# Performance work log

Measured on AMD Instinct MI355X. Metric: run time of the kernel, lower is better.

The kernel has to match this reference:

```python
import jax, jax.numpy as jnp
import numpy as np

N_NODES = 50000
NEG_SLOPE = 0.2


def gat_layer(x, src, dst, edge_attr, W, a_src, a_dst, We, a_edge, b, n):
    """PyG GATConv (heads=1, concat=True, add_self_loops=True, fill_value='mean')."""
    h = x @ W                                   # [N, C] shared lin for src/dst
    alpha_s = h @ a_src                          # [N]
    alpha_d = h @ a_dst                          # [N]
    # self loops; self-loop edge_attr = mean of incoming edge_attr per node
    deg = jax.ops.segment_sum(jnp.ones_like(dst, dtype=edge_attr.dtype), dst, num_segments=n)
    ea_mean = jax.ops.segment_sum(edge_attr, dst, num_segments=n) / jnp.maximum(deg, 1.0)[:, None]
    loop = jnp.arange(n, dtype=src.dtype)
    s = jnp.concatenate([src, loop])             # [E+N]
    d = jnp.concatenate([dst, loop])
    ea = jnp.concatenate([edge_attr, ea_mean], axis=0)
    alpha_e = (ea @ We) @ a_edge                 # [E+N]
    alpha = jax.nn.leaky_relu(alpha_s[s] + alpha_d[d] + alpha_e, NEG_SLOPE)
    # segment softmax over destination neighborhoods (self-loops guarantee non-empty)
    amax = jax.ops.segment_max(alpha, d, num_segments=n)
    ealpha = jnp.exp(alpha - amax[d])
    denom = jax.ops.segment_sum(ealpha, d, num_segments=n)
    coef = ealpha / denom[d]                     # [E+N]
    out = jax.ops.segment_sum(h[s] * coef[:, None], d, num_segments=n)
    return out + b


def setup_inputs() -> dict:
    key = jax.random.key(0)
    ks = jax.random.split(key, 16)
    N, E, F_in, H, C, ED = N_NODES, 800000, 256, 128, 128, 60
    inp = {
        "x": jax.random.normal(ks[0], (N, F_in), jnp.float32),
        "edge_index": jax.random.randint(ks[1], (2, E), 0, N, jnp.int32),
        "edge_features": jax.random.normal(ks[2], (E, ED), jnp.float32),
        "batch_size": 16,
    }
    def glorot(k, shape):
        fan = shape[0] + (shape[1] if len(shape) > 1 else 1)
        return jax.random.normal(k, shape, jnp.float32) * np.sqrt(2.0 / fan)
    # layer 1
    inp["W1"] = glorot(ks[3], (F_in, H))
    inp["a_src1"] = glorot(ks[4], (H,))
    inp["a_dst1"] = glorot(ks[5], (H,))
    inp["We1"] = glorot(ks[6], (ED, H))
    inp["a_edge1"] = glorot(ks[7], (H,))
    inp["b1"] = jnp.zeros((H,), jnp.float32)
    # layer 2
    inp["W2"] = glorot(ks[8], (H, C))
    inp["a_src2"] = glorot(ks[9], (C,))
    inp["a_dst2"] = glorot(ks[10], (C,))
    inp["We2"] = glorot(ks[11], (ED, C))
    inp["a_edge2"] = glorot(ks[12], (C,))
    inp["b2"] = jnp.zeros((C,), jnp.float32)
    return inp


def reference(x, edge_index, edge_features, batch_size,
              W1, a_src1, a_dst1, We1, a_edge1, b1,
              W2, a_src2, a_dst2, We2, a_edge2, b2):
    n = x.shape[0]
    src, dst = edge_index[0], edge_index[1]
    h = gat_layer(x, src, dst, edge_features, W1, a_src1, a_dst1, We1, a_edge1, b1, n)
    h = jax.nn.relu(h)
    z = gat_layer(h, src, dst, edge_features, W2, a_src2, a_dst2, We2, a_edge2, b2, n)
    # decode: gather-dot over labeled edge pairs
    res = jnp.sum(z[src] * z[dst], axis=-1)      # [E]
    half = res.shape[0] // 2
    res_half = res[:half] + res[half:]
    return res_half.reshape((batch_size, -1))
```

## Files before the change

### kernel.cpp

```cpp
#include <hip/hip_runtime.h>
#include <hip/hip_bf16.h>

typedef __attribute__((ext_vector_type(8))) short short8;
typedef __attribute__((ext_vector_type(4))) float floatx4;

__device__ __forceinline__ float wsum(float v){
  #pragma unroll
  for (int m = 32; m >= 1; m >>= 1) v += __shfl_xor(v, m);
  return v;
}
__device__ __forceinline__ float lrelu(float a){ return a > 0.f ? a : 0.2f * a; }
__device__ __forceinline__ float bflo(unsigned u){ return __uint_as_float(u << 16); }
__device__ __forceinline__ float bfhi(unsigned u){ return __uint_as_float(u & 0xffff0000u); }
__device__ __forceinline__ unsigned short f2bf(float f){
  __hip_bfloat16 h = __float2bfloat16(f);
  return *reinterpret_cast<unsigned short*>(&h);
}

__global__ __launch_bounds__(256) void k_prep(const float* __restrict__ We1, const float* __restrict__ ae1,
                       const float* __restrict__ We2, const float* __restrict__ ae2,
                       float* __restrict__ we1, float* __restrict__ we2,
                       const float* __restrict__ W1, unsigned short* __restrict__ W1t,
                       const float* __restrict__ W2, unsigned short* __restrict__ W2t) {
  int b = blockIdx.x, t = threadIdx.x;
  if (b == 0) {
    if (t >= 64) return;
    float s1 = 0.f, s2 = 0.f;
    if (t < 60) {
      const float4* r1 = reinterpret_cast<const float4*>(We1 + t * 128);
      const float4* r2 = reinterpret_cast<const float4*>(We2 + t * 128);
      const float4* a1 = reinterpret_cast<const float4*>(ae1);
      const float4* a2 = reinterpret_cast<const float4*>(ae2);
      for (int i = 0; i < 32; ++i) {
        float4 x1 = r1[i], y1 = a1[i];
        float4 x2 = r2[i], y2 = a2[i];
        s1 += x1.x*y1.x + x1.y*y1.y + x1.z*y1.z + x1.w*y1.w;
        s2 += x2.x*y2.x + x2.y*y2.y + x2.z*y2.z + x2.w*y2.w;
      }
    }
    we1[t] = s1; we2[t] = s2;
  } else if (b <= 128) {
    int idx = (b - 1) * 256 + t;
    int k = idx >> 7, n = idx & 127;
    W1t[(size_t)n * 256 + k] = f2bf(W1[idx]);
  } else {
    int idx = (b - 129) * 256 + t;
    int k = idx >> 7, n = idx & 127;
    W2t[(size_t)n * 128 + k] = f2bf(W2[idx]);
  }
}

__global__ void k_count(const int* __restrict__ dst, int* __restrict__ degi,
                        int* __restrict__ eslot, int E) {
  int e = blockIdx.x * blockDim.x + threadIdx.x;
  if (e < E) eslot[e] = atomicAdd(degi + dst[e], 1);
}

__global__ __launch_bounds__(1024) void k_scan(const int* __restrict__ degi, int* __restrict__ rowptr,
                                               int N, int E) {
  __shared__ int part[1024];
  int t = threadIdx.x;
  const int CH = 52;
  int lo = t * CH;
  int v[52];
  int s = 0;
  #pragma unroll
  for (int i = 0; i < 13; ++i) {
    int base_i = lo + 4 * i;
    if (base_i + 4 <= N) {
      int4 q = *reinterpret_cast<const int4*>(degi + base_i);
      v[4*i+0] = q.x; v[4*i+1] = q.y; v[4*i+2] = q.z; v[4*i+3] = q.w;
      s += q.x + q.y + q.z + q.w;
    } else {
      #pragma unroll
      for (int j = 0; j < 4; ++j) {
        int idx = base_i + j;
        int x = (idx < N) ? degi[idx] : 0;
        v[4*i+j] = x; s += x;
      }
    }
  }
  part[t] = s;
  __syncthreads();
  for (int off = 1; off < 1024; off <<= 1) {
    int u = (t >= off) ? part[t - off] : 0;
    __syncthreads();
    part[t] += u;
    __syncthreads();
  }
  int base = (t == 0) ? 0 : part[t - 1];
  #pragma unroll
  for (int i = 0; i < 13; ++i) {
    int base_i = lo + 4 * i;
    if (base_i + 4 <= N) {
      int4 o;
      o.x = base; base += v[4*i+0];
      o.y = base; base += v[4*i+1];
      o.z = base; base += v[4*i+2];
      o.w = base; base += v[4*i+3];
      *reinterpret_cast<int4*>(rowptr + base_i) = o;
    } else {
      #pragma unroll
      for (int j = 0; j < 4; ++j) {
        int idx = base_i + j;
        if (idx < N) { rowptr[idx] = base; base += v[4*i+j]; }
      }
    }
  }
  if (t == 0) rowptr[N] = E;
}

__global__ __launch_bounds__(256) void k_fill(const int* __restrict__ src, const int* __restrict__ dst,
                       const float* __restrict__ ef,
                       const float* __restrict__ we1, const float* __restrict__ we2,
                       const int* __restrict__ rowptr, const int* __restrict__ eslot,
                       float4* __restrict__ csr, int E) {
  __shared__ float w1[64], w2[64];
  int t = threadIdx.x;
  if (t < 64) { w1[t] = we1[t]; w2[t] = we2[t]; }
  __syncthreads();
  int gid = blockIdx.x * 256 + t;
  int e = gid >> 2;
  int sub = gid & 3;
  if (e >= E) return;
  const float4* row = reinterpret_cast<const float4*>(ef + (size_t)e * 60);
  float d1 = 0.f, d2 = 0.f;
  #pragma unroll
  for (int i = sub; i < 15; i += 4) {
    float4 f = row[i];
    d1 += f.x*w1[4*i] + f.y*w1[4*i+1] + f.z*w1[4*i+2] + f.w*w1[4*i+3];
    d2 += f.x*w2[4*i] + f.y*w2[4*i+1] + f.z*w2[4*i+2] + f.w*w2[4*i+3];
  }
  d1 += __shfl_xor(d1, 1); d1 += __shfl_xor(d1, 2);
  d2 += __shfl_xor(d2, 1); d2 += __shfl_xor(d2, 2);
  if (sub == 0) {
    int d = dst[e];
    int slot = rowptr[d] + eslot[e];
    float4 v;
    v.x = __int_as_float(src[e]); v.y = d1; v.z = d2; v.w = 0.f;
    csr[slot] = v;
  }
}

template <int K, bool AFP32>
__global__ __launch_bounds__(256) void k_gemm(const void* __restrict__ Av, const unsigned short* __restrict__ Bt,
                                              unsigned short* __restrict__ C, int M) {
  int wid = (blockIdx.x * 256 + threadIdx.x) >> 6;
  int lane = threadIdx.x & 63;
  int mt = wid >> 1, hf = wid & 1;
  if (mt * 16 >= M) return;
  int r = lane & 15, quad = lane >> 4;
  int m = mt * 16 + r;
  floatx4 acc[4] = {};
  for (int k0 = 0; k0 < K; k0 += 32) {
    int kk = k0 + quad * 8;
    short8 a;
    if (AFP32) {
      const float4* ap = reinterpret_cast<const float4*>((const float*)Av + (size_t)m * K + kk);
      float4 lo = ap[0], hi = ap[1];
      union { short8 v; unsigned short u[8]; } pa;
      pa.u[0]=f2bf(lo.x); pa.u[1]=f2bf(lo.y); pa.u[2]=f2bf(lo.z); pa.u[3]=f2bf(lo.w);
      pa.u[4]=f2bf(hi.x); pa.u[5]=f2bf(hi.y); pa.u[6]=f2bf(hi.z); pa.u[7]=f2bf(hi.w);
      a = pa.v;
    } else {
      a = *reinterpret_cast<const short8*>((const unsigned short*)Av + (size_t)m * K + kk);
    }
    #pragma unroll
    for (int t = 0; t < 4; ++t) {
      short8 b = *reinterpret_cast<const short8*>(Bt + (size_t)(hf*64 + t*16 + r) * K + kk);
      acc[t] = __builtin_amdgcn_mfma_f32_16x16x32_bf16(a, b, acc[t], 0, 0, 0);
    }
  }
  #pragma unroll
  for (int t = 0; t < 4; ++t) {
    int col = hf * 64 + t * 16 + r;
    #pragma unroll
    for (int rr = 0; rr < 4; ++rr) {
      int row = mt * 16 + quad * 4 + rr;
      C[(size_t)row * 128 + col] = f2bf(acc[t][rr]);
    }
  }
}

__global__ void k_alpha(const unsigned short* __restrict__ h,
                        const float* __restrict__ a_src, const float* __restrict__ a_dst,
                        float* __restrict__ as_, float* __restrict__ ad_, int N) {
  int wave = (blockIdx.x * blockDim.x + threadIdx.x) >> 6;
  int lane = threadIdx.x & 63;
  if (wave >= N) return;
  unsigned u = *reinterpret_cast<const unsigned*>(h + (size_t)wave * 128 + lane * 2);
  float f0 = bflo(u), f1 = bfhi(u);
  float2 sv = reinterpret_cast<const float2*>(a_src)[lane];
  float2 dv = reinterpret_cast<const float2*>(a_dst)[lane];
  float ps = f0 * sv.x + f1 * sv.y;
  float pd = f0 * dv.x + f1 * dv.y;
  ps = wsum(ps);
  pd = wsum(pd);
  if (lane == 0) { as_[wave] = ps; ad_[wave] = pd; }
}

__global__ __launch_bounds__(256) void k_agg(const int* __restrict__ rowptr, const float4* __restrict__ csr,
                      const float* __restrict__ as_, const float* __restrict__ ad_,
                      const unsigned short* __restrict__ h, const float* __restrict__ bias,
                      unsigned short* __restrict__ out, int N, int use2, int do_relu) {
  int i = (blockIdx.x * blockDim.x + threadIdx.x) >> 6;
  int lane = threadIdx.x & 63;
  if (i >= N) return;
  int st = lane >> 4;
  int q  = lane & 15;
  int start = rowptr[i], end = rowptr[i + 1];
  int cnt = end - start;
  float adi = ad_[i], asi = as_[i];
  float m = -3.0e38f, s = 0.f, esum = 0.f;
  float acc[8] = {};
  int idx = start + st;
  float4 cur;
  if (idx < end) cur = csr[idx];
  for (; idx < end; idx += 4) {
    int nidx = idx + 4;
    float4 nxt;
    if (nidx < end) nxt = csr[nidx];
    int sv = __float_as_int(cur.x);
    float e = use2 ? cur.z : cur.y;
    float a = lrelu(as_[sv] + adi + e);
    esum += e;
    if (a > m) {
      float r = __expf(m - a);
      s *= r;
      #pragma unroll
      for (int j = 0; j < 8; ++j) acc[j] *= r;
      m = a;
    }
    float w = __expf(a - m);
    s += w;
    uint4 hv = *reinterpret_cast<const uint4*>(h + (size_t)sv * 128 + q * 8);
    acc[0] += w * bflo(hv.x); acc[1] += w * bfhi(hv.x);
    acc[2] += w * bflo(hv.y); acc[3] += w * bfhi(hv.y);
    acc[4] += w * bflo(hv.z); acc[5] += w * bfhi(hv.z);
    acc[6] += w * bflo(hv.w); acc[7] += w * bfhi(hv.w);
    cur = nxt;
  }
  #pragma unroll
  for (int off = 16; off <= 32; off <<= 1) {
    float m_o = __shfl_xor(m, off);
    float s_o = __shfl_xor(s, off);
    float e_o = __shfl_xor(esum, off);
    float ao[8];
    #pragma unroll
    for (int j = 0; j < 8; ++j) ao[j] = __shfl_xor(acc[j], off);
    float Mn = fmaxf(m, m_o);
    float f  = __expf(m - Mn), fo = __expf(m_o - Mn);
    s = s * f + s_o * fo;
    #pragma unroll
    for (int j = 0; j < 8; ++j) acc[j] = acc[j] * f + ao[j] * fo;
    esum += e_o;
    m = Mn;
  }
  float a_self = lrelu(asi + adi + esum / fmaxf((float)cnt, 1.f));
  float M2 = fmaxf(m, a_self);
  float g = __expf(m - M2);
  float w_self = __expf(a_self - M2);
  s = s * g + w_self;
  uint4 hs = *reinterpret_cast<const uint4*>(h + (size_t)i * 128 + q * 8);
  float hsf[8] = { bflo(hs.x), bfhi(hs.x), bflo(hs.y), bfhi(hs.y),
                   bflo(hs.z), bfhi(hs.z), bflo(hs.w), bfhi(hs.w) };
  #pragma unroll
  for (int j = 0; j < 8; ++j) acc[j] = acc[j] * g + w_self * hsf[j];
  float inv = 1.0f / s;
  float4 bv0 = *reinterpret_cast<const float4*>(bias + q * 8);
  float4 bv1 = *reinterpret_cast<const float4*>(bias + q * 8 + 4);
  float o[8];
  o[0] = acc[0]*inv + bv0.x; o[1] = acc[1]*inv + bv0.y;
  o[2] = acc[2]*inv + bv0.z; o[3] = acc[3]*inv + bv0.w;
  o[4] = acc[4]*inv + bv1.x; o[5] = acc[5]*inv + bv1.y;
  o[6] = acc[6]*inv + bv1.z; o[7] = acc[7]*inv + bv1.w;
  if (do_relu) {
    #pragma unroll
    for (int j = 0; j < 8; ++j) o[j] = fmaxf(o[j], 0.f);
  }
  if (st == 0) {
    uint4 ov;
    ov.x = (unsigned)f2bf(o[0]) | ((unsigned)f2bf(o[1]) << 16);
    ov.y = (unsigned)f2bf(o[2]) | ((unsigned)f2bf(o[3]) << 16);
    ov.z = (unsigned)f2bf(o[4]) | ((unsigned)f2bf(o[5]) << 16);
    ov.w = (unsigned)f2bf(o[6]) | ((unsigned)f2bf(o[7]) << 16);
    *reinterpret_cast<uint4*>(out + (size_t)i * 128 + q * 8) = ov;
  }
}

__global__ void k_decode(const int* __restrict__ src, const int* __restrict__ dst,
                         const unsigned short* __restrict__ z, float* __restrict__ out, int halfE) {
  int w = (blockIdx.x * blockDim.x + threadIdx.x) >> 6;
  int lane = threadIdx.x & 63;
  int k0 = w * 4;
  if (k0 >= halfE) return;
  int hh = lane >> 5, q = lane & 31;
  float p[4];
  #pragma unroll
  for (int r = 0; r < 4; ++r) {
    p[r] = 0.f;
    int k = k0 + r;
    if (k < halfE) {
      int e = k + hh * halfE;
      int sv = src[e], dv = dst[e];
      uint2 a = *reinterpret_cast<const uint2*>(z + (size_t)sv * 128 + q * 4);
      uint2 b = *reinterpret_cast<const uint2*>(z + (size_t)dv * 128 + q * 4);
      p[r] = bflo(a.x)*bflo(b.x) + bfhi(a.x)*bfhi(b.x)
           + bflo(a.y)*bflo(b.y) + bfhi(a.y)*bfhi(b.y);
    }
  }
  #pragma unroll
  for (int r = 0; r < 4; ++r) p[r] = wsum(p[r]);
  if (lane == 0) {
    if (k0 + 4 <= halfE) {
      float4 ov = make_float4(p[0], p[1], p[2], p[3]);
      *reinterpret_cast<float4*>(out + k0) = ov;
    } else {
      for (int r = 0; r < 4 && k0 + r < halfE; ++r) out[k0 + r] = p[r];
    }
  }
}

extern "C" void kernel_launch(void* const* d_in, const int* in_sizes, int n_in,
                              void* d_out, int out_size, void* d_ws, size_t ws_size,
                              hipStream_t stream) {
  const int H = 128;
  const int N = in_sizes[0] / 256;
  const int E = in_sizes[1] / 2;
  const int half = E / 2;

  const float* x   = (const float*)d_in[0];
  const int* eidx  = (const int*)d_in[1];
  const float* ef  = (const float*)d_in[2];
  const float* W1  = (const float*)d_in[4];
  const float* as1 = (const float*)d_in[5];
  const float* ad1 = (const float*)d_in[6];
  const float* We1 = (const float*)d_in[7];
  const float* ae1 = (const float*)d_in[8];
  const float* b1  = (const float*)d_in[9];
  const float* W2  = (const float*)d_in[10];
  const float* as2 = (const float*)d_in[11];
  const float* ad2 = (const float*)d_in[12];
  const float* We2 = (const float*)d_in[13];
  const float* ae2 = (const float*)d_in[14];
  const float* b2  = (const float*)d_in[15];

  const int* src = eidx;
  const int* dst = eidx + E;

  size_t off = 0;
  auto alloc = [&](size_t bytes) -> void* {
    void* p = (char*)d_ws + off;
    off += (bytes + 255) & ~(size_t)255;
    return p;
  };
  float*  we1    = (float*)alloc(64 * 4);
  float*  we2    = (float*)alloc(64 * 4);
  int*    degi   = (int*)alloc((size_t)N * 4);
  int*    eslot  = (int*)alloc((size_t)E * 4);
  int*    rowptr = (int*)alloc((size_t)(N + 1) * 4);
  float*  alps   = (float*)alloc((size_t)N * 4);
  float*  alpd   = (float*)alloc((size_t)N * 4);
  float4* csr    = (float4*)alloc((size_t)E * 16);
  unsigned short* W1t = (unsigned short*)alloc((size_t)128 * 256 * 2);
  unsigned short* W2t = (unsigned short*)alloc((size_t)128 * 128 * 2);
  unsigned short* hA  = (unsigned short*)alloc((size_t)N * H * 2);
  unsigned short* hB  = (unsigned short*)alloc((size_t)N * H * 2);

  hipMemsetAsync(degi, 0, (size_t)N * 4, stream);

  k_prep<<<193, 256, 0, stream>>>(We1, ae1, We2, ae2, we1, we2, W1, W1t, W2, W2t);
  k_count<<<(E + 255) / 256, 256, 0, stream>>>(dst, degi, eslot, E);
  k_scan<<<1, 1024, 0, stream>>>(degi, rowptr, N, E);
  k_fill<<<(E * 4 + 255) / 256, 256, 0, stream>>>(src, dst, ef, we1, we2, rowptr, eslot, csr, E);

  int gwaves = ((N + 15) / 16) * 2;
  int gblocks = (gwaves + 3) / 4;
  k_gemm<256, true><<<gblocks, 256, 0, stream>>>(x, W1t, hA, N);
  k_alpha<<<(N + 3) / 4, 256, 0, stream>>>(hA, as1, ad1, alps, alpd, N);
  k_agg<<<(N + 3) / 4, 256, 0, stream>>>(rowptr, csr, alps, alpd, hA, b1, hB, N, 0, 1);
  k_gemm<128, false><<<gblocks, 256, 0, stream>>>(hB, W2t, hA, N);
  k_alpha<<<(N + 3) / 4, 256, 0, stream>>>(hA, as2, ad2, alps, alpd, N);
  k_agg<<<(N + 3) / 4, 256, 0, stream>>>(rowptr, csr, alps, alpd, hA, b2, hB, N, 1, 0);
  int dwaves = (half + 3) / 4;
  k_decode<<<(dwaves + 3) / 4, 256, 0, stream>>>(src, dst, hB, (float*)d_out, half);
}
```

Measured before the change: 619.9 us.

## Fuse alpha projection into GEMM epilogue, prefetch gathers in aggregation, widen decode loads

New measurement: 591.4 us. 4.6% less time.

```diff
diff --git a/kernel.cpp b/kernel.cpp
--- a/kernel.cpp
+++ b/kernel.cpp
@@ -144,7 +144,9 @@
 
 template <int K, bool AFP32>
 __global__ __launch_bounds__(256) void k_gemm(const void* __restrict__ Av, const unsigned short* __restrict__ Bt,
-                                              unsigned short* __restrict__ C, int M) {
+                                              unsigned short* __restrict__ C,
+                                              const float* __restrict__ a_src, const float* __restrict__ a_dst,
+                                              float* __restrict__ alps, float* __restrict__ alpd, int M) {
   int wid = (blockIdx.x * 256 + threadIdx.x) >> 6;
   int lane = threadIdx.x & 63;
   int mt = wid >> 1, hf = wid & 1;
@@ -171,6 +173,25 @@
       acc[t] = __builtin_amdgcn_mfma_f32_16x16x32_bf16(a, b, acc[t], 0, 0, 0);
     }
   }
+  float asv[4], adv[4];
+  #pragma unroll
+  for (int t = 0; t < 4; ++t) {
+    int col = hf * 64 + t * 16 + r;
+    asv[t] = a_src[col]; adv[t] = a_dst[col];
+  }
+  #pragma unroll
+  for (int rr = 0; rr < 4; ++rr) {
+    float ps = 0.f, pd = 0.f;
+    #pragma unroll
+    for (int t = 0; t < 4; ++t) { ps += acc[t][rr] * asv[t]; pd += acc[t][rr] * adv[t]; }
+    #pragma unroll
+    for (int mo = 1; mo <= 8; mo <<= 1) { ps += __shfl_xor(ps, mo); pd += __shfl_xor(pd, mo); }
+    if (r == 0) {
+      int row = mt * 16 + quad * 4 + rr;
+      atomicAdd(alps + row, ps);
+      atomicAdd(alpd + row, pd);
+    }
+  }
   #pragma unroll
   for (int t = 0; t < 4; ++t) {
     int col = hf * 64 + t * 16 + r;
@@ -180,23 +201,6 @@
       C[(size_t)row * 128 + col] = f2bf(acc[t][rr]);
     }
   }
-}
-
-__global__ void k_alpha(const unsigned short* __restrict__ h,
-                        const float* __restrict__ a_src, const float* __restrict__ a_dst,
-                        float* __restrict__ as_, float* __restrict__ ad_, int N) {
-  int wave = (blockIdx.x * blockDim.x + threadIdx.x) >> 6;
-  int lane = threadIdx.x & 63;
-  if (wave >= N) return;
-  unsigned u = *reinterpret_cast<const unsigned*>(h + (size_t)wave * 128 + lane * 2);
-  float f0 = bflo(u), f1 = bfhi(u);
-  float2 sv = reinterpret_cast<const float2*>(a_src)[lane];
-  float2 dv = reinterpret_cast<const float2*>(a_dst)[lane];
-  float ps = f0 * sv.x + f1 * sv.y;
-  float pd = f0 * dv.x + f1 * dv.y;
-  ps = wsum(ps);
-  pd = wsum(pd);
-  if (lane == 0) { as_[wave] = ps; ad_[wave] = pd; }
 }
 
 __global__ __launch_bounds__(256) void k_agg(const int* __restrict__ rowptr, const float4* __restrict__ csr,
@@ -214,31 +218,41 @@
   float m = -3.0e38f, s = 0.f, esum = 0.f;
   float acc[8] = {};
   int idx = start + st;
-  float4 cur;
-  if (idx < end) cur = csr[idx];
+  float4 cur, nx;
+  float as_c = 0.f; uint4 hv_c;
+  if (idx < end) {
+    cur = csr[idx];
+    int sv = __float_as_int(cur.x);
+    as_c = as_[sv];
+    hv_c = *reinterpret_cast<const uint4*>(h + (size_t)sv * 128 + q * 8);
+  }
+  if (idx + 4 < end) nx = csr[idx + 4];
   for (; idx < end; idx += 4) {
-    int nidx = idx + 4;
-    float4 nxt;
-    if (nidx < end) nxt = csr[nidx];
-    int sv = __float_as_int(cur.x);
+    float4 n2;
+    if (idx + 8 < end) n2 = csr[idx + 8];
+    float as_n = 0.f; uint4 hv_n;
+    if (idx + 4 < end) {
+      int svn = __float_as_int(nx.x);
+      as_n = as_[svn];
+      hv_n = *reinterpret_cast<const uint4*>(h + (size_t)svn * 128 + q * 8);
+    }
     float e = use2 ? cur.z : cur.y;
-    float a = lrelu(as_[sv] + adi + e);
+    float a = lrelu(as_c + adi + e);
     esum += e;
-    if (a > m) {
-      float r = __expf(m - a);
-      s *= r;
+    if (a > m + 8.f) {
+      float rr = __expf(m - a);
+      s *= rr;
       #pragma unroll
-      for (int j = 0; j < 8; ++j) acc[j] *= r;
+      for (int j = 0; j < 8; ++j) acc[j] *= rr;
       m = a;
     }
     float w = __expf(a - m);
     s += w;
-    uint4 hv = *reinterpret_cast<const uint4*>(h + (size_t)sv * 128 + q * 8);
-    acc[0] += w * bflo(hv.x); acc[1] += w * bfhi(hv.x);
-    acc[2] += w * bflo(hv.y); acc[3] += w * bfhi(hv.y);
-    acc[4] += w * bflo(hv.z); acc[5] += w * bfhi(hv.z);
-    acc[6] += w * bflo(hv.w); acc[7] += w * bfhi(hv.w);
-    cur = nxt;
+    acc[0] += w * bflo(hv_c.x); acc[1] += w * bfhi(hv_c.x);
+    acc[2] += w * bflo(hv_c.y); acc[3] += w * bfhi(hv_c.y);
+    acc[4] += w * bflo(hv_c.z); acc[5] += w * bfhi(hv_c.z);
+    acc[6] += w * bflo(hv_c.w); acc[7] += w * bfhi(hv_c.w);
+    cur = nx; nx = n2; as_c = as_n; hv_c = hv_n;
   }
   #pragma unroll
   for (int off = 16; off <= 32; off <<= 1) {
@@ -292,31 +306,30 @@
                          const unsigned short* __restrict__ z, float* __restrict__ out, int halfE) {
   int w = (blockIdx.x * blockDim.x + threadIdx.x) >> 6;
   int lane = threadIdx.x & 63;
-  int k0 = w * 4;
+  int k0 = w * 2;
   if (k0 >= halfE) return;
-  int hh = lane >> 5, q = lane & 31;
-  float p[4];
-  #pragma unroll
-  for (int r = 0; r < 4; ++r) {
-    p[r] = 0.f;
-    int k = k0 + r;
-    if (k < halfE) {
-      int e = k + hh * halfE;
-      int sv = src[e], dv = dst[e];
-      uint2 a = *reinterpret_cast<const uint2*>(z + (size_t)sv * 128 + q * 4);
-      uint2 b = *reinterpret_cast<const uint2*>(z + (size_t)dv * 128 + q * 4);
-      p[r] = bflo(a.x)*bflo(b.x) + bfhi(a.x)*bfhi(b.x)
-           + bflo(a.y)*bflo(b.y) + bfhi(a.y)*bfhi(b.y);
-    }
-  }
-  #pragma unroll
-  for (int r = 0; r < 4; ++r) p[r] = wsum(p[r]);
+  int sel = lane >> 4;
+  int q = lane & 15;
+  int k = k0 + (sel >> 1), hh = sel & 1;
+  float p = 0.f;
+  if (k < halfE) {
+    int e = k + hh * halfE;
+    int sv = src[e], dv = dst[e];
+    uint4 a = *reinterpret_cast<const uint4*>(z + (size_t)sv * 128 + q * 8);
+    uint4 b = *reinterpret_cast<const uint4*>(z + (size_t)dv * 128 + q * 8);
+    p = bflo(a.x)*bflo(b.x) + bfhi(a.x)*bfhi(b.x)
+      + bflo(a.y)*bflo(b.y) + bfhi(a.y)*bfhi(b.y)
+      + bflo(a.z)*bflo(b.z) + bfhi(a.z)*bfhi(b.z)
+      + bflo(a.w)*bflo(b.w) + bfhi(a.w)*bfhi(b.w);
+  }
+  #pragma unroll
+  for (int mo = 1; mo <= 16; mo <<= 1) p += __shfl_xor(p, mo);
+  float p1 = __shfl(p, 32);
   if (lane == 0) {
-    if (k0 + 4 <= halfE) {
-      float4 ov = make_float4(p[0], p[1], p[2], p[3]);
-      *reinterpret_cast<float4*>(out + k0) = ov;
+    if (k0 + 2 <= halfE) {
+      *reinterpret_cast<float2*>(out + k0) = make_float2(p, p1);
     } else {
-      for (int r = 0; r < 4 && k0 + r < halfE; ++r) out[k0 + r] = p[r];
+      out[k0] = p;
     }
   }
 }
@@ -356,18 +369,21 @@
   };
   float*  we1    = (float*)alloc(64 * 4);
   float*  we2    = (float*)alloc(64 * 4);
-  int*    degi   = (int*)alloc((size_t)N * 4);
+  int*    zeroblk= (int*)alloc((size_t)N * 4 * 5);
+  int*    degi   = zeroblk;
+  float*  alps1  = (float*)(zeroblk + (size_t)N);
+  float*  alpd1  = (float*)(zeroblk + (size_t)2 * N);
+  float*  alps2  = (float*)(zeroblk + (size_t)3 * N);
+  float*  alpd2  = (float*)(zeroblk + (size_t)4 * N);
   int*    eslot  = (int*)alloc((size_t)E * 4);
   int*    rowptr = (int*)alloc((size_t)(N + 1) * 4);
-  float*  alps   = (float*)alloc((size_t)N * 4);
-  float*  alpd   = (float*)alloc((size_t)N * 4);
   float4* csr    = (float4*)alloc((size_t)E * 16);
   unsigned short* W1t = (unsigned short*)alloc((size_t)128 * 256 * 2);
   unsigned short* W2t = (unsigned short*)alloc((size_t)128 * 128 * 2);
   unsigned short* hA  = (unsigned short*)alloc((size_t)N * H * 2);
   unsigned short* hB  = (unsigned short*)alloc((size_t)N * H * 2);
 
-  hipMemsetAsync(degi, 0, (size_t)N * 4, stream);
+  hipMemsetAsync(zeroblk, 0, (size_t)N * 4 * 5, stream);
 
   k_prep<<<193, 256, 0, stream>>>(We1, ae1, We2, ae2, we1, we2, W1, W1t, W2, W2t);
   k_count<<<(E + 255) / 256, 256, 0, stream>>>(dst, degi, eslot, E);
@@ -376,12 +392,10 @@
 
   int gwaves = ((N + 15) / 16) * 2;
   int gblocks = (gwaves + 3) / 4;
-  k_gemm<256, true><<<gblocks, 256, 0, stream>>>(x, W1t, hA, N);
-  k_alpha<<<(N + 3) / 4, 256, 0, stream>>>(hA, as1, ad1, alps, alpd, N);
-  k_agg<<<(N + 3) / 4, 256, 0, stream>>>(rowptr, csr, alps, alpd, hA, b1, hB, N, 0, 1);
-  k_gemm<128, false><<<gblocks, 256, 0, stream>>>(hB, W2t, hA, N);
-  k_alpha<<<(N + 3) / 4, 256, 0, stream>>>(hA, as2, ad2, alps, alpd, N);
-  k_agg<<<(N + 3) / 4, 256, 0, stream>>>(rowptr, csr, alps, alpd, hA, b2, hB, N, 1, 0);
-  int dwaves = (half + 3) / 4;
+  k_gemm<256, true><<<gblocks, 256, 0, stream>>>(x, W1t, hA, as1, ad1, alps1, alpd1, N);
+  k_agg<<<(N + 3) / 4, 256, 0, stream>>>(rowptr, csr, alps1, alpd1, hA, b1, hB, N, 0, 1);
+  k_gemm<128, false><<<gblocks, 256, 0, stream>>>(hB, W2t, hA, as2, ad2, alps2, alpd2, N);
+  k_agg<<<(N + 3) / 4, 256, 0, stream>>>(rowptr, csr, alps2, alpd2, hA, b2, hB, N, 1, 0);
+  int dwaves = (half + 1) / 2;
   k_decode<<<(dwaves + 3) / 4, 256, 0, stream>>>(src, dst, hB, (float*)d_out, half);
 }
```
